# Performance work log

Hardware: AMD Instinct MI355X
Metric: run time of the kernel (lower is better)

The kernel has to match this reference:

```python
import jax, jax.numpy as jnp
import numpy as np

THR = 1.0
ALPHA = 5.0
C = 0.4
TAU_U = 20.0
DT = 1.0

def slayer(x):
    # SE-adlif SLAYER surrogate: c*alpha / (2*exp(alpha*|x|))
    return C * ALPHA / (2.0 * jnp.exp(jnp.abs(x) * ALPHA))

def setup_inputs() -> dict:
    key = jax.random.key(0)
    k1, k2, k3 = jax.random.split(key, 3)
    B, T, IN, OUT = 64, 1000, 512, 512
    x = jax.random.normal(k1, (B, T, IN), dtype=jnp.float32)
    lim = 1.0 / np.sqrt(IN)
    weight = jax.random.uniform(k2, (OUT, IN), minval=-lim, maxval=lim, dtype=jnp.float32)
    bias = jnp.zeros((OUT,), jnp.float32)
    # orthogonal init for recurrent weights
    recurrent = jnp.linalg.qr(jax.random.normal(k3, (OUT, OUT), dtype=jnp.float32))[0].astype(jnp.float32)
    # fixed tau trainer: decay = exp(-dt/tau)
    decay = jnp.full((OUT,), np.exp(-DT / TAU_U), dtype=jnp.float32)
    return {"input_tensor": x, "weight": weight, "bias": bias, "recurrent": recurrent, "decay": decay}

def reference(input_tensor, weight, bias, recurrent, decay):
    B = input_tensor.shape[0]
    OUT = weight.shape[0]
    sg = jax.lax.stop_gradient
    # precompute input-driven current for all timesteps: [B, T, OUT]
    cur = jnp.einsum('bti,oi->bto', input_tensor, weight) + bias
    v0 = jnp.zeros((B, OUT), jnp.float32)
    z0 = jnp.zeros((B, OUT), jnp.float32)

    def step(carry, c_t):
        v_tm1, z_tm1 = carry
        v_tm1 = v_tm1 * (1.0 - sg(z_tm1))  # detached reset
        soma = c_t + z_tm1 @ recurrent.T
        v_t = decay * v_tm1 + (1.0 - decay) * soma
        v_thr = v_t - THR
        hv = jnp.where(v_thr >= 0, 1.0, 0.0).astype(v_thr.dtype)
        # straight-through: value = heaviside, grad = SLAYER surrogate
        z_t = sg(hv) + (v_thr - sg(v_thr)) * sg(slayer(v_thr))
        return (v_t, z_t), (v_t, z_t)

    _, (vs, zs) = jax.lax.scan(step, (v0, z0), jnp.swapaxes(cur, 0, 1))
    vs = jnp.swapaxes(vs, 0, 1)  # [B, T, OUT]
    zs = jnp.swapaxes(zs, 0, 1)
    v_full = jnp.concatenate([v0[:, None], vs], axis=1)  # [B, T+1, OUT]
    z_full = jnp.concatenate([z0[:, None], zs], axis=1)
    states = jnp.stack([v_full, z_full], axis=0)  # [2, B, T+1, OUT]
    outputs = zs  # [B, T, OUT]
    return outputs, states
```

## Files before the change

kernel.cpp:

```cpp
#include <hip/hip_runtime.h>
#include <hip/hip_bf16.h>

#define SV_OFF 32768000
#define SZ_OFF 65568768

typedef __attribute__((ext_vector_type(8))) short bf16x8;
typedef __attribute__((ext_vector_type(4))) float f32x4;

__device__ __forceinline__ unsigned short f2bf(float f) {
  union { float f; unsigned u; } x; x.f = f;
  unsigned r = x.u + 0x7fffu + ((x.u >> 16) & 1u);
  return (unsigned short)(r >> 16);
}

__device__ __forceinline__ void gl_lds16(const void* g, void* l) {
  __builtin_amdgcn_global_load_lds(
      (const __attribute__((address_space(1))) unsigned int*)g,
      (__attribute__((address_space(3))) unsigned int*)l, 16, 0, 0);
}

__global__ __launch_bounds__(256) void prep(const float* __restrict__ W,
                                            const float* __restrict__ R,
                                            unsigned short* __restrict__ Wb,
                                            float* __restrict__ RT,
                                            int* __restrict__ flags) {
  const int idx = blockIdx.x * 256 + threadIdx.x;
  if (idx < 512 * 512) {
    Wb[idx] = f2bf(W[idx]);
    const int j = idx >> 9;
    const int o = idx & 511;
    RT[idx] = R[o * 512 + j];
  }
  if (idx < 64) flags[idx] = 0;
}

__global__ __launch_bounds__(256, 2) void gemm_cur(
    const float* __restrict__ A,
    const unsigned short* __restrict__ Wb,
    const float* __restrict__ bias,
    float* __restrict__ C) {
  __shared__ unsigned short As[128][40];
  __shared__ unsigned short Bs[128][32];
  const int tid = threadIdx.x;
  const int bn = blockIdx.x * 128;
  const int bm = blockIdx.y * 128;
  const int wave = tid >> 6;
  const int lane = tid & 63;
  const int lr = lane & 15;
  const int lq = lane >> 4;
  const int mh = (wave & 1) * 64;
  const int nh = (wave >> 1) * 64;

  f32x4 acc[4][4] = {};

  const int arow = tid >> 3;
  const int acol = (tid & 7) * 4;
  const int ldsoff0 = tid * 16;

  for (int kk = 0; kk < 16; ++kk) {
    const int k0 = kk * 32;
    __syncthreads();
#pragma unroll
    for (int p = 0; p < 4; ++p) {
      const int r = arow + p * 32;
      const float4 a4 = *(const float4*)(A + (size_t)(bm + r) * 512 + k0 + acol);
      ushort4 h;
      h.x = f2bf(a4.x); h.y = f2bf(a4.y); h.z = f2bf(a4.z); h.w = f2bf(a4.w);
      *(ushort4*)(&As[r][acol]) = h;
    }
#pragma unroll
    for (int q = 0; q < 2; ++q) {
      const int lo = q * 4096 + ldsoff0;
      const int row = lo >> 6;
      const int kb = lo & 63;
      gl_lds16((const char*)Wb + (size_t)(bn + row) * 1024 + (size_t)k0 * 2 + kb,
               (char*)(&Bs[0][0]) + lo);
    }
    __syncthreads();
    bf16x8 af[4], bfr[4];
#pragma unroll
    for (int i = 0; i < 4; ++i)
      af[i] = *(const bf16x8*)(&As[mh + i * 16 + lr][lq * 8]);
#pragma unroll
    for (int j = 0; j < 4; ++j)
      bfr[j] = *(const bf16x8*)(&Bs[nh + j * 16 + lr][lq * 8]);
#pragma unroll
    for (int i = 0; i < 4; ++i)
#pragma unroll
      for (int j = 0; j < 4; ++j)
        acc[i][j] = __builtin_amdgcn_mfma_f32_16x16x32_bf16(af[i], bfr[j], acc[i][j], 0, 0, 0);
  }
#pragma unroll
  for (int j = 0; j < 4; ++j) {
    const int col = bn + nh + j * 16 + lr;
    const float bv = bias[col];
#pragma unroll
    for (int i = 0; i < 4; ++i) {
      const int r0 = bm + mh + i * 16 + lq * 4;
#pragma unroll
      for (int r = 0; r < 4; ++r)
        C[(size_t)(r0 + r) * 512 + col] = acc[i][j][r] + bv;
    }
  }
}

__global__ __launch_bounds__(64) void scan_spec(const float* __restrict__ cur,
                                                const float* __restrict__ decay,
                                                float* __restrict__ out,
                                                int* __restrict__ flags) {
  const int b = blockIdx.x >> 3;
  const int o = ((blockIdx.x & 7) << 6) + threadIdx.x;
  const float d = decay[o];
  const float om = 1.0f - d;
  float v = 0.f, z = 0.f;
  int fl = 0;
  const size_t ci = (size_t)b * 512000 + o;
  const size_t svb = (size_t)b * 512512 + o;
  float* __restrict__ sv = out + SV_OFF;
  float* __restrict__ sz = out + SZ_OFF;
  sv[svb] = 0.f;
  sz[svb] = 0.f;
  float nb[8];
#pragma unroll
  for (int u = 0; u < 8; ++u) nb[u] = cur[ci + (size_t)u * 512];
  for (int t = 0; t < 1000; t += 8) {
    float cb[8];
#pragma unroll
    for (int u = 0; u < 8; ++u) cb[u] = nb[u];
    if (t + 8 < 1000) {
      const size_t p = ci + (size_t)(t + 8) * 512;
#pragma unroll
      for (int u = 0; u < 8; ++u) nb[u] = cur[p + (size_t)u * 512];
    }
#pragma unroll
    for (int u = 0; u < 8; ++u) {
      v = d * (v * (1.f - z)) + om * cb[u];
      z = (v >= 1.0f) ? 1.0f : 0.0f;
      fl |= (v >= 1.0f);
      const size_t row = (size_t)(t + u) * 512;
      out[ci + row] = z;
      sv[svb + row + 512] = v;
      sz[svb + row + 512] = z;
    }
  }
  if (fl) atomicOr(flags + b, 1);
}

__global__ __launch_bounds__(512) void scan_fix(const float* __restrict__ cur,
                                                const float* __restrict__ decay,
                                                const float* __restrict__ RT,
                                                float* __restrict__ out,
                                                const int* __restrict__ flags) {
  const int b = blockIdx.x;
  if (flags[b] == 0) return;
  const int o = threadIdx.x;
  __shared__ int cnt;
  __shared__ int list[512];
  const float d = decay[o];
  const float om = 1.f - d;
  float v = 0.f, z = 0.f;
  const size_t ci = (size_t)b * 512000 + o;
  const size_t svb = (size_t)b * 512512 + o;
  float* __restrict__ sv = out + SV_OFF;
  float* __restrict__ sz = out + SZ_OFF;
  sv[svb] = 0.f;
  sz[svb] = 0.f;
  if (o == 0) cnt = 0;
  __syncthreads();
  for (int t = 0; t < 1000; ++t) {
    float soma = cur[ci + (size_t)t * 512];
    const int n = cnt;
    for (int i = 0; i < n; ++i) soma += RT[(size_t)list[i] * 512 + o];
    v = d * (v * (1.f - z)) + om * soma;
    z = (v >= 1.0f) ? 1.0f : 0.0f;
    out[ci + (size_t)t * 512] = z;
    sv[svb + (size_t)(t + 1) * 512] = v;
    sz[svb + (size_t)(t + 1) * 512] = z;
    __syncthreads();
    if (o == 0) cnt = 0;
    __syncthreads();
    if (z != 0.f) { const int p = atomicAdd(&cnt, 1); list[p] = o; }
    __syncthreads();
  }
}

extern "C" void kernel_launch(void* const* d_in, const int* in_sizes, int n_in,
                              void* d_out, int out_size, void* d_ws, size_t ws_size,
                              hipStream_t stream) {
  (void)in_sizes; (void)n_in; (void)out_size; (void)ws_size;
  const float* x     = (const float*)d_in[0];
  const float* W     = (const float*)d_in[1];
  const float* bias  = (const float*)d_in[2];
  const float* R     = (const float*)d_in[3];
  const float* decay = (const float*)d_in[4];
  float* out = (float*)d_out;

  char* ws = (char*)d_ws;
  float* cur          = (float*)ws;
  unsigned short* Wb  = (unsigned short*)(ws + 131072000);
  float* RT           = (float*)(ws + 131596288);
  int* flags          = (int*)(ws + 132644864);

  prep<<<1024, 256, 0, stream>>>(W, R, Wb, RT, flags);
  gemm_cur<<<dim3(4, 500), 256, 0, stream>>>(x, Wb, bias, cur);
  scan_spec<<<512, 64, 0, stream>>>(cur, decay, out, flags);
  scan_fix<<<64, 512, 0, stream>>>(cur, decay, RT, out, flags);
}
```

Before: 646.3 us.

## Split speculative no-spike scan into parallel time chunks with prefix carry

The sequential per-neuron scan over 1000 steps becomes a three-pass chunked linear scan: chunk_sums computes each 125-step chunk's decayed sum, chunk_prefix combines the chunks, and chunk_scan replays each chunk from its carried-in state. This exposes 8x more threads, so the latency-bound serial loop becomes shorter and better at hiding memory latency. Because the speculative path assumes no spikes, the reset term is dropped and any spike still sets the flag that sends that batch to scan_fix. Output stores now use nontemporal hints. The cost is an extra full read of cur and two more launches.

```diff
diff --git a/kernel.cpp b/kernel.cpp
--- a/kernel.cpp
+++ b/kernel.cpp
@@ -3,6 +3,8 @@
 
 #define SV_OFF 32768000
 #define SZ_OFF 65568768
+#define TC 125
+#define NC 8
 
 typedef __attribute__((ext_vector_type(8))) short bf16x8;
 typedef __attribute__((ext_vector_type(4))) float f32x4;
@@ -104,44 +106,81 @@
   }
 }
 
-__global__ __launch_bounds__(64) void scan_spec(const float* __restrict__ cur,
-                                                const float* __restrict__ decay,
-                                                float* __restrict__ out,
-                                                int* __restrict__ flags) {
-  const int b = blockIdx.x >> 3;
-  const int o = ((blockIdx.x & 7) << 6) + threadIdx.x;
+__global__ __launch_bounds__(256) void chunk_sums(const float* __restrict__ cur,
+                                                  const float* __restrict__ decay,
+                                                  float* __restrict__ S) {
+  const int gt = blockIdx.x * 256 + threadIdx.x;
+  const int o = gt & 511;
+  const int j = (gt >> 9) & (NC - 1);
+  const int b = gt >> 12;
   const float d = decay[o];
   const float om = 1.0f - d;
-  float v = 0.f, z = 0.f;
-  int fl = 0;
-  const size_t ci = (size_t)b * 512000 + o;
-  const size_t svb = (size_t)b * 512512 + o;
+  const size_t base = (size_t)b * 512000 + (size_t)(j * TC) * 512 + o;
+  float nb[8];
+#pragma unroll
+  for (int u = 0; u < 8; ++u) nb[u] = cur[base + (size_t)u * 512];
+  float s = 0.f;
+#pragma unroll 8
+  for (int k = 0; k < TC; ++k) {
+    const float c = nb[k & 7];
+    if (k < TC - 8) nb[k & 7] = cur[base + (size_t)(k + 8) * 512];
+    s = d * s + om * c;
+  }
+  S[gt] = s;
+}
+
+__global__ __launch_bounds__(256) void chunk_prefix(const float* __restrict__ S,
+                                                    const float* __restrict__ decay,
+                                                    float* __restrict__ Vs) {
+  const int gt = blockIdx.x * 256 + threadIdx.x;
+  const int o = gt & 511;
+  const int b = gt >> 9;
+  const float d = decay[o];
+  const float dTC = powf(d, (float)TC);
+  float v = 0.f;
+  const int base = (b << 12) + o;
+#pragma unroll
+  for (int j = 0; j < NC; ++j) {
+    Vs[base + (j << 9)] = v;
+    v = dTC * v + S[base + (j << 9)];
+  }
+}
+
+__global__ __launch_bounds__(256) void chunk_scan(const float* __restrict__ cur,
+                                                  const float* __restrict__ decay,
+                                                  const float* __restrict__ Vs,
+                                                  float* __restrict__ out,
+                                                  int* __restrict__ flags) {
+  const int gt = blockIdx.x * 256 + threadIdx.x;
+  const int o = gt & 511;
+  const int j = (gt >> 9) & (NC - 1);
+  const int b = gt >> 12;
+  const float d = decay[o];
+  const float om = 1.0f - d;
+  const size_t ci = (size_t)b * 512000 + (size_t)(j * TC) * 512 + o;
+  const size_t svb = (size_t)b * 512512 + (size_t)(j * TC) * 512 + o;
   float* __restrict__ sv = out + SV_OFF;
   float* __restrict__ sz = out + SZ_OFF;
-  sv[svb] = 0.f;
-  sz[svb] = 0.f;
+  if (j == 0) {
+    __builtin_nontemporal_store(0.f, &sv[svb]);
+    __builtin_nontemporal_store(0.f, &sz[svb]);
+  }
+  float v = Vs[(b << 12) + (j << 9) + o];
+  int fl = 0;
   float nb[8];
 #pragma unroll
   for (int u = 0; u < 8; ++u) nb[u] = cur[ci + (size_t)u * 512];
-  for (int t = 0; t < 1000; t += 8) {
-    float cb[8];
-#pragma unroll
-    for (int u = 0; u < 8; ++u) cb[u] = nb[u];
-    if (t + 8 < 1000) {
-      const size_t p = ci + (size_t)(t + 8) * 512;
-#pragma unroll
-      for (int u = 0; u < 8; ++u) nb[u] = cur[p + (size_t)u * 512];
-    }
-#pragma unroll
-    for (int u = 0; u < 8; ++u) {
-      v = d * (v * (1.f - z)) + om * cb[u];
-      z = (v >= 1.0f) ? 1.0f : 0.0f;
-      fl |= (v >= 1.0f);
-      const size_t row = (size_t)(t + u) * 512;
-      out[ci + row] = z;
-      sv[svb + row + 512] = v;
-      sz[svb + row + 512] = z;
-    }
+#pragma unroll 8
+  for (int k = 0; k < TC; ++k) {
+    const float c = nb[k & 7];
+    if (k < TC - 8) nb[k & 7] = cur[ci + (size_t)(k + 8) * 512];
+    v = d * v + om * c;
+    const float z = (v >= 1.0f) ? 1.0f : 0.0f;
+    fl |= (v >= 1.0f);
+    const size_t row = (size_t)k * 512;
+    __builtin_nontemporal_store(z, &out[ci + row]);
+    __builtin_nontemporal_store(v, &sv[svb + row + 512]);
+    __builtin_nontemporal_store(z, &sz[svb + row + 512]);
   }
   if (fl) atomicOr(flags + b, 1);
 }
@@ -200,9 +239,13 @@
   unsigned short* Wb  = (unsigned short*)(ws + 131072000);
   float* RT           = (float*)(ws + 131596288);
   int* flags          = (int*)(ws + 132644864);
+  float* S            = (float*)(ws + 132648960);
+  float* Vs           = (float*)(ws + 133697536);
 
   prep<<<1024, 256, 0, stream>>>(W, R, Wb, RT, flags);
   gemm_cur<<<dim3(4, 500), 256, 0, stream>>>(x, Wb, bias, cur);
-  scan_spec<<<512, 64, 0, stream>>>(cur, decay, out, flags);
+  chunk_sums<<<1024, 256, 0, stream>>>(cur, decay, S);
+  chunk_prefix<<<128, 256, 0, stream>>>(S, decay, Vs);
+  chunk_scan<<<1024, 256, 0, stream>>>(cur, decay, Vs, out, flags);
   scan_fix<<<64, 512, 0, stream>>>(cur, decay, RT, out, flags);
 }
```

Measured after the change: 618.6 us. -4.3%, faster.
